# Kernel optimization log

Measured on AMD Instinct MI355X. Metric: run time of the kernel, lower is better.

## Reference

```python
import jax, jax.numpy as jnp
import numpy as np
import math

WIDTH = 1024
NUM_HEADS = 16
HEAD_DIM = WIDTH // NUM_HEADS
WINDOW_SIZE = 256
MIN_LOGITS_VALUE = -1e30


def setup_inputs() -> dict:
    key = jax.random.key(0)
    ks = jax.random.split(key, 7)
    b, t = 2, 2048
    std = math.sqrt(1.0 / WIDTH)
    x = jax.random.normal(ks[0], (b, t, WIDTH), dtype=jnp.float32)
    segment_pos = jnp.broadcast_to(jnp.arange(t, dtype=jnp.int32)[None, :], (b, t))
    Wq = jax.random.normal(ks[1], (WIDTH, WIDTH), dtype=jnp.float32) * std
    Wk = jax.random.normal(ks[2], (HEAD_DIM, WIDTH), dtype=jnp.float32) * std
    Wv = jax.random.normal(ks[3], (HEAD_DIM, WIDTH), dtype=jnp.float32) * std
    Wf = jax.random.normal(ks[4], (WIDTH, WIDTH), dtype=jnp.float32) * std
    bf = jnp.zeros((WIDTH,), dtype=jnp.float32)
    return {"x": x, "segment_pos": segment_pos, "Wq": Wq, "Wk": Wk, "Wv": Wv, "Wf": Wf, "bf": bf}


def reference(x, segment_pos, Wq, Wk, Wv, Wf, bf):
    b, t, _ = x.shape
    # projections (Linear: x @ W.T)
    q = (x @ Wq.T).reshape(b, t, NUM_HEADS, HEAD_DIM)  # [b,t,n,h]
    k = x @ Wk.T  # [b,t,h] single shared KV head (MQA)
    v = x @ Wv.T  # [b,t,h]
    scale = 1.0 / math.sqrt(HEAD_DIM)
    logits = jnp.einsum('btnh,bsh->bnts', q, k) * scale  # [b,n,t,s]
    # sliding-window causal mask: q_pos >= k_pos and q_pos <= k_pos + window
    ar = jnp.arange(t)
    qp = ar[:, None]
    kp = ar[None, :]
    mask = (qp >= kp) & (qp <= kp + WINDOW_SIZE)  # [t,s]
    masked = jnp.where(mask[None, None, :, :], logits, MIN_LOGITS_VALUE)
    probs = jax.nn.softmax(masked.astype(jnp.float32), axis=-1).astype(logits.dtype)
    out = jnp.einsum('bnts,bsh->btnh', probs, v)  # [b,t,n,h]
    out = out.reshape(b, t, WIDTH)
    return out @ Wf.T + bf
```

## Files before the change

### kernel.cpp

```cpp
#include <hip/hip_runtime.h>
#include <stdint.h>

#define B_SZ   2
#define T_SEQ  2048
#define WIDTH_ 1024
#define NH     16
#define HD     64
#define WIN    256
#define MROWS  (B_SZ * T_SEQ)
#define NQKV   1152

typedef __attribute__((ext_vector_type(4))) float f32x4;
typedef __attribute__((ext_vector_type(8))) short s16x8;

typedef __attribute__((address_space(1))) const void gas_void;
typedef __attribute__((address_space(3))) void las_void;

#define MFMA(a, b, c) __builtin_amdgcn_mfma_f32_16x16x32_bf16((a), (b), (c), 0, 0, 0)

__device__ __forceinline__ void gload_lds16(const void* g, void* l) {
  __builtin_amdgcn_global_load_lds((gas_void*)g, (las_void*)l, 16, 0, 0);
}

__device__ __forceinline__ ushort f2bf(float f) {
  union { float f; uint32_t u; } v; v.f = f;
  uint32_t u = v.u;
  return (ushort)((u + 0x7FFFu + ((u >> 16) & 1u)) >> 16);
}

__global__ void prep_kernel(const float* __restrict__ x,
                            const float* __restrict__ Wq,
                            const float* __restrict__ Wk,
                            const float* __restrict__ Wv,
                            const float* __restrict__ Wf,
                            ushort* __restrict__ xb,
                            ushort* __restrict__ wqkv,
                            ushort* __restrict__ wfb) {
  const int XN = MROWS * WIDTH_ / 4;
  const int WQ = NQKV * WIDTH_ / 4;
  const int WF = WIDTH_ * WIDTH_ / 4;
  int i = blockIdx.x * blockDim.x + threadIdx.x;
  float4 v;
  ushort* dst;
  if (i < XN) {
    v = ((const float4*)x)[i];
    dst = xb + i * 4;
  } else if (i < XN + WQ) {
    int j = i - XN;
    int row = (j * 4) >> 10;
    int col = (j * 4) & 1023;
    const float* src = (row < 1024) ? (Wq + row * 1024 + col)
                     : (row < 1088) ? (Wk + (row - 1024) * 1024 + col)
                                    : (Wv + (row - 1088) * 1024 + col);
    v = *(const float4*)src;
    dst = wqkv + j * 4;
  } else if (i < XN + WQ + WF) {
    int j = i - XN - WQ;
    v = ((const float4*)Wf)[j];
    dst = wfb + j * 4;
  } else {
    return;
  }
  ushort4 o;
  o.x = f2bf(v.x); o.y = f2bf(v.y); o.z = f2bf(v.z); o.w = f2bf(v.w);
  *(ushort4*)dst = o;
}

#define G_STAGE(AS, BS, KOFF) do {                                          \
  _Pragma("unroll")                                                         \
  for (int i_ = 0; i_ < 2; ++i_) {                                          \
    int c_ = i_ * 256 + w * 64 + lane;                                      \
    int row_ = c_ >> 2;                                                     \
    int ke_ = (c_ & 3) * 8;                                                 \
    int ldsb_ = (i_ * 256 + w * 64) * 16;                                   \
    gload_lds16(A + (size_t)(m0 + row_) * 1024 + (KOFF) + ke_,              \
                (char*)(AS) + ldsb_);                                       \
    gload_lds16(B + (size_t)(n0 + row_) * 1024 + (KOFF) + ke_,              \
                (char*)(BS) + ldsb_);                                       \
  }                                                                         \
} while (0)

#define G_COMPUTE(AS, BS) do {                                              \
  s16x8 af_[4], bf_[4];                                                     \
  _Pragma("unroll")                                                         \
  for (int t_ = 0; t_ < 4; ++t_) {                                          \
    af_[t_] = *(const s16x8*)&(AS)[(wm + t_ * 16 + r16) * 32 + g * 8];      \
    bf_[t_] = *(const s16x8*)&(BS)[(wn + t_ * 16 + r16) * 32 + g * 8];      \
  }                                                                         \
  _Pragma("unroll")                                                         \
  for (int mb_ = 0; mb_ < 4; ++mb_)                                         \
    _Pragma("unroll")                                                       \
    for (int nb_ = 0; nb_ < 4; ++nb_)                                       \
      acc[mb_][nb_] = MFMA(af_[mb_], bf_[nb_], acc[mb_][nb_]);              \
} while (0)

template <int MODE>
__global__ __launch_bounds__(256) void gemm_kernel(
    const ushort* __restrict__ A, const ushort* __restrict__ B,
    ushort* __restrict__ qb, ushort* __restrict__ kb, ushort* __restrict__ vt,
    float* __restrict__ Cf, const float* __restrict__ bias) {
  const int w = threadIdx.x >> 6;
  const int lane = threadIdx.x & 63;
  const int g = lane >> 4;
  const int r16 = lane & 15;
  const int m0 = blockIdx.y * 128;
  const int n0 = blockIdx.x * 128;
  const int wm = (w >> 1) * 64;
  const int wn = (w & 1) * 64;

  __shared__ ushort As0[128 * 32];
  __shared__ ushort Bs0[128 * 32];
  __shared__ ushort As1[128 * 32];
  __shared__ ushort Bs1[128 * 32];

  f32x4 acc[4][4] = {};

  G_STAGE(As0, Bs0, 0);
  for (int k0 = 0; k0 < 1024; k0 += 64) {
    __syncthreads();
    G_STAGE(As1, Bs1, k0 + 32);
    G_COMPUTE(As0, Bs0);
    __syncthreads();
    if (k0 + 64 < 1024) G_STAGE(As0, Bs0, k0 + 64);
    G_COMPUTE(As1, Bs1);
  }

#pragma unroll
  for (int mb = 0; mb < 4; ++mb)
#pragma unroll
    for (int nb = 0; nb < 4; ++nb) {
      int n = n0 + wn + nb * 16 + r16;
      int mbase = m0 + wm + mb * 16 + 4 * g;
      if (MODE == 0) {
#pragma unroll
        for (int r = 0; r < 4; ++r) {
          ushort h = f2bf(acc[mb][nb][r]);
          int m = mbase + r;
          if (n < 1024)      qb[m * 1024 + n] = h;
          else if (n < 1088) kb[m * 64 + (n - 1024)] = h;
          else               vt[((size_t)((m >> 11) * 64 + (n - 1088))) * 2048 +
                                (m & 2047)] = h;
        }
      } else {
        float bv = bias[n];
#pragma unroll
        for (int r = 0; r < 4; ++r)
          Cf[(size_t)(mbase + r) * 1024 + n] = acc[mb][nb][r] + bv;
      }
    }
}

__global__ __launch_bounds__(64) void attn_kernel(
    const ushort* __restrict__ qb, const ushort* __restrict__ kb,
    const ushort* __restrict__ vt, ushort* __restrict__ ao) {
  const int lane = threadIdx.x;
  const int g = lane >> 4;
  const int r16 = lane & 15;
  const int blk = blockIdx.x;
  const int qt = blk & 63;
  const int h = (blk >> 6) & 15;
  const int b = blk >> 10;
  const int q0 = qt * 32;
  const int qpA = q0 + r16;
  const int qpB = q0 + 16 + r16;

  const ushort* qrowA = qb + (size_t)(b * 2048 + qpA) * 1024 + h * 64;
  const ushort* qrowB = qb + (size_t)(b * 2048 + qpB) * 1024 + h * 64;
  s16x8 qfA0 = *(const s16x8*)(qrowA + g * 8);
  s16x8 qfA1 = *(const s16x8*)(qrowA + 32 + g * 8);
  s16x8 qfB0 = *(const s16x8*)(qrowB + g * 8);
  s16x8 qfB1 = *(const s16x8*)(qrowB + 32 + g * 8);

  f32x4 oaccA[4] = {}, oaccB[4] = {};
  float mA = -1e30f, lA = 0.f, mB = -1e30f, lB = 0.f;

  int kt0 = q0 - WIN;
  if (kt0 < 0) kt0 = 0;
  kt0 &= ~31;

  s16x8 k00, k01, k10, k11;
  {
    const ushort* kp0 = kb + (size_t)(b * 2048 + kt0 + r16) * 64;
    const ushort* kp1 = kb + (size_t)(b * 2048 + kt0 + 16 + r16) * 64;
    k00 = *(const s16x8*)(kp0 + g * 8);
    k01 = *(const s16x8*)(kp0 + 32 + g * 8);
    k10 = *(const s16x8*)(kp1 + g * 8);
    k11 = *(const s16x8*)(kp1 + 32 + g * 8);
  }

  for (int kt = kt0; kt <= q0; kt += 32) {
    s16x8 c00 = k00, c01 = k01, c10 = k10, c11 = k11;
    if (kt + 32 <= q0) {
      const ushort* kp0 = kb + (size_t)(b * 2048 + kt + 32 + r16) * 64;
      const ushort* kp1 = kb + (size_t)(b * 2048 + kt + 48 + r16) * 64;
      k00 = *(const s16x8*)(kp0 + g * 8);
      k01 = *(const s16x8*)(kp0 + 32 + g * 8);
      k10 = *(const s16x8*)(kp1 + g * 8);
      k11 = *(const s16x8*)(kp1 + 32 + g * 8);
    }

    f32x4 sA0 = {}, sA1 = {}, sB0 = {}, sB1 = {};
    sA0 = MFMA(c00, qfA0, sA0); sA0 = MFMA(c01, qfA1, sA0);
    sA1 = MFMA(c10, qfA0, sA1); sA1 = MFMA(c11, qfA1, sA1);
    sB0 = MFMA(c00, qfB0, sB0); sB0 = MFMA(c01, qfB1, sB0);
    sB1 = MFMA(c10, qfB0, sB1); sB1 = MFMA(c11, qfB1, sB1);

    float pA0[4], pA1[4], pB0[4], pB1[4];
    float tmA = -1e30f, tmB = -1e30f;
#pragma unroll
    for (int r = 0; r < 4; ++r) {
      int ka = kt + 4 * g + r;
      int kc = ka + 16;
      float a0 = (ka <= qpA && qpA - ka <= WIN) ? sA0[r] * 0.125f : -1e30f;
      float a1 = (kc <= qpA && qpA - kc <= WIN) ? sA1[r] * 0.125f : -1e30f;
      float b0 = (ka <= qpB && qpB - ka <= WIN) ? sB0[r] * 0.125f : -1e30f;
      float b1 = (kc <= qpB && qpB - kc <= WIN) ? sB1[r] * 0.125f : -1e30f;
      pA0[r] = a0; pA1[r] = a1; pB0[r] = b0; pB1[r] = b1;
      tmA = fmaxf(tmA, fmaxf(a0, a1));
      tmB = fmaxf(tmB, fmaxf(b0, b1));
    }
    tmA = fmaxf(tmA, __shfl_xor(tmA, 16));
    tmA = fmaxf(tmA, __shfl_xor(tmA, 32));
    tmB = fmaxf(tmB, __shfl_xor(tmB, 16));
    tmB = fmaxf(tmB, __shfl_xor(tmB, 32));

    float mnA = fmaxf(mA, tmA), mnB = fmaxf(mB, tmB);
    float corrA = __expf(mA - mnA), corrB = __expf(mB - mnB);
    float tsA = 0.f, tsB = 0.f;
    s16x8 pfA, pfB;
#pragma unroll
    for (int r = 0; r < 4; ++r) {
      float eA0 = __expf(pA0[r] - mnA);
      float eA1 = __expf(pA1[r] - mnA);
      float eB0 = __expf(pB0[r] - mnB);
      float eB1 = __expf(pB1[r] - mnB);
      tsA += eA0 + eA1; tsB += eB0 + eB1;
      pfA[r] = (short)f2bf(eA0); pfA[4 + r] = (short)f2bf(eA1);
      pfB[r] = (short)f2bf(eB0); pfB[4 + r] = (short)f2bf(eB1);
    }
    tsA += __shfl_xor(tsA, 16); tsA += __shfl_xor(tsA, 32);
    tsB += __shfl_xor(tsB, 16); tsB += __shfl_xor(tsB, 32);
    lA = lA * corrA + tsA; mA = mnA;
    lB = lB * corrB + tsB; mB = mnB;

#pragma unroll
    for (int db = 0; db < 4; ++db) { oaccA[db] *= corrA; oaccB[db] *= corrB; }

#pragma unroll
    for (int db = 0; db < 4; ++db) {
      const ushort* vrow = vt + (size_t)(b * 64 + db * 16 + r16) * 2048 + kt;
      ushort4 va = *(const ushort4*)(vrow + 4 * g);
      ushort4 vc = *(const ushort4*)(vrow + 16 + 4 * g);
      s16x8 vf;
      vf[0] = (short)va.x; vf[1] = (short)va.y; vf[2] = (short)va.z; vf[3] = (short)va.w;
      vf[4] = (short)vc.x; vf[5] = (short)vc.y; vf[6] = (short)vc.z; vf[7] = (short)vc.w;
      oaccA[db] = MFMA(vf, pfA, oaccA[db]);
      oaccB[db] = MFMA(vf, pfB, oaccB[db]);
    }
  }

  float invA = 1.0f / lA, invB = 1.0f / lB;
  ushort* orowA = ao + (size_t)(b * 2048 + qpA) * 1024 + h * 64;
  ushort* orowB = ao + (size_t)(b * 2048 + qpB) * 1024 + h * 64;
#pragma unroll
  for (int db = 0; db < 4; ++db) {
    ushort4 oA, oB;
    oA.x = f2bf(oaccA[db][0] * invA); oA.y = f2bf(oaccA[db][1] * invA);
    oA.z = f2bf(oaccA[db][2] * invA); oA.w = f2bf(oaccA[db][3] * invA);
    oB.x = f2bf(oaccB[db][0] * invB); oB.y = f2bf(oaccB[db][1] * invB);
    oB.z = f2bf(oaccB[db][2] * invB); oB.w = f2bf(oaccB[db][3] * invB);
    *(ushort4*)(orowA + db * 16 + 4 * g) = oA;
    *(ushort4*)(orowB + db * 16 + 4 * g) = oB;
  }
}

extern "C" void kernel_launch(void* const* d_in, const int* in_sizes, int n_in,
                              void* d_out, int out_size, void* d_ws, size_t ws_size,
                              hipStream_t stream) {
  const float* x  = (const float*)d_in[0];
  const float* Wq = (const float*)d_in[2];
  const float* Wk = (const float*)d_in[3];
  const float* Wv = (const float*)d_in[4];
  const float* Wf = (const float*)d_in[5];
  const float* bf = (const float*)d_in[6];
  float* out = (float*)d_out;

  uint8_t* w8 = (uint8_t*)d_ws;
  ushort* xb   = (ushort*)(w8 + 0);
  ushort* qbuf = (ushort*)(w8 + 8388608);
  ushort* attn = (ushort*)(w8 + 16777216);
  ushort* wqkv = (ushort*)(w8 + 25165824);
  ushort* wfb  = (ushort*)(w8 + 27525120);
  ushort* kbuf = (ushort*)(w8 + 29622272);
  ushort* vt   = (ushort*)(w8 + 30146560);

  prep_kernel<<<6272, 256, 0, stream>>>(x, Wq, Wk, Wv, Wf, xb, wqkv, wfb);
  gemm_kernel<0><<<dim3(9, 32), 256, 0, stream>>>(xb, wqkv, qbuf, kbuf, vt,
                                                  nullptr, nullptr);
  attn_kernel<<<2048, 64, 0, stream>>>(qbuf, kbuf, vt, attn);
  gemm_kernel<1><<<dim3(8, 32), 256, 0, stream>>>(attn, wfb, nullptr, nullptr,
                                                  nullptr, out, bf);
}
```

Before: 158.6 us.

## Shrink GEMM tiles to 64x64 with XCD swizzle, hoist V loads and set MFMA priority

The GEMM tile shrinks from 128x128 to 64x64 and uses a 1D grid whose block index is remapped across the 8 XCDs. This is meant to give the small M=4096 GEMMs enough workgroups to fill the device. An explicit vmcnt(0) wait is added before each barrier so the global-to-LDS loads are complete before use. In attention, the V fragments are loaded at the top of each iteration so their latency overlaps the QK MFMAs and softmax, and s_setprio brackets the MFMA blocks. Smaller tiles reduce data reuse per block and double global traffic per FLOP.

```diff
diff --git a/kernel.cpp b/kernel.cpp
--- a/kernel.cpp
+++ b/kernel.cpp
@@ -17,6 +17,8 @@
 typedef __attribute__((address_space(3))) void las_void;
 
 #define MFMA(a, b, c) __builtin_amdgcn_mfma_f32_16x16x32_bf16((a), (b), (c), 0, 0, 0)
+
+#define VMEM_DRAIN() asm volatile("s_waitcnt vmcnt(0)" ::: "memory")
 
 __device__ __forceinline__ void gload_lds16(const void* g, void* l) {
   __builtin_amdgcn_global_load_lds((gas_void*)g, (las_void*)l, 16, 0, 0);
@@ -67,30 +69,27 @@
 }
 
 #define G_STAGE(AS, BS, KOFF) do {                                          \
+  int c_ = w * 64 + lane;                                       \
+  int row_ = c_ >> 2;                                                       \
+  int ke_ = (c_ & 3) * 8;                                                   \
+  int ldsb_ = c_ * 16;                     \
+  gload_lds16(A + (size_t)(m0 + row_) * 1024 + (KOFF) + ke_,                \
+              (char*)(AS) + ldsb_);                                         \
+  gload_lds16(B + (size_t)(n0 + row_) * 1024 + (KOFF) + ke_,                \
+              (char*)(BS) + ldsb_);                                         \
+} while (0)
+
+#define G_COMPUTE(AS, BS) do {                                              \
+  s16x8 af_[2], bf_[2];                                                     \
   _Pragma("unroll")                                                         \
-  for (int i_ = 0; i_ < 2; ++i_) {                                          \
-    int c_ = i_ * 256 + w * 64 + lane;                                      \
-    int row_ = c_ >> 2;                                                     \
-    int ke_ = (c_ & 3) * 8;                                                 \
-    int ldsb_ = (i_ * 256 + w * 64) * 16;                                   \
-    gload_lds16(A + (size_t)(m0 + row_) * 1024 + (KOFF) + ke_,              \
-                (char*)(AS) + ldsb_);                                       \
-    gload_lds16(B + (size_t)(n0 + row_) * 1024 + (KOFF) + ke_,              \
-                (char*)(BS) + ldsb_);                                       \
-  }                                                                         \
-} while (0)
-
-#define G_COMPUTE(AS, BS) do {                                              \
-  s16x8 af_[4], bf_[4];                                                     \
-  _Pragma("unroll")                                                         \
-  for (int t_ = 0; t_ < 4; ++t_) {                                          \
+  for (int t_ = 0; t_ < 2; ++t_) {                                          \
     af_[t_] = *(const s16x8*)&(AS)[(wm + t_ * 16 + r16) * 32 + g * 8];      \
     bf_[t_] = *(const s16x8*)&(BS)[(wn + t_ * 16 + r16) * 32 + g * 8];      \
   }                                                                         \
   _Pragma("unroll")                                                         \
-  for (int mb_ = 0; mb_ < 4; ++mb_)                                         \
+  for (int mb_ = 0; mb_ < 2; ++mb_)                                         \
     _Pragma("unroll")                                                       \
-    for (int nb_ = 0; nb_ < 4; ++nb_)                                       \
+    for (int nb_ = 0; nb_ < 2; ++nb_)                                       \
       acc[mb_][nb_] = MFMA(af_[mb_], bf_[nb_], acc[mb_][nb_]);              \
 } while (0)
 
@@ -99,36 +98,45 @@
     const ushort* __restrict__ A, const ushort* __restrict__ B,
     ushort* __restrict__ qb, ushort* __restrict__ kb, ushort* __restrict__ vt,
     float* __restrict__ Cf, const float* __restrict__ bias) {
+  const int NBX = (MODE == 0) ? 18 : 16;
+  const int nwg = NBX * 64;
+  const int cpx = nwg >> 3;
+  int swz = (blockIdx.x & 7) * cpx + (blockIdx.x >> 3);
+  const int bx = swz % NBX;
+  const int by = swz / NBX;
+
   const int w = threadIdx.x >> 6;
   const int lane = threadIdx.x & 63;
   const int g = lane >> 4;
   const int r16 = lane & 15;
-  const int m0 = blockIdx.y * 128;
-  const int n0 = blockIdx.x * 128;
-  const int wm = (w >> 1) * 64;
-  const int wn = (w & 1) * 64;
-
-  __shared__ ushort As0[128 * 32];
-  __shared__ ushort Bs0[128 * 32];
-  __shared__ ushort As1[128 * 32];
-  __shared__ ushort Bs1[128 * 32];
-
-  f32x4 acc[4][4] = {};
+  const int m0 = by * 64;
+  const int n0 = bx * 64;
+  const int wm = (w >> 1) * 32;
+  const int wn = (w & 1) * 32;
+
+  __shared__ ushort As0[64 * 32];
+  __shared__ ushort Bs0[64 * 32];
+  __shared__ ushort As1[64 * 32];
+  __shared__ ushort Bs1[64 * 32];
+
+  f32x4 acc[2][2] = {};
 
   G_STAGE(As0, Bs0, 0);
   for (int k0 = 0; k0 < 1024; k0 += 64) {
+    VMEM_DRAIN();
     __syncthreads();
     G_STAGE(As1, Bs1, k0 + 32);
     G_COMPUTE(As0, Bs0);
+    VMEM_DRAIN();
     __syncthreads();
     if (k0 + 64 < 1024) G_STAGE(As0, Bs0, k0 + 64);
     G_COMPUTE(As1, Bs1);
   }
 
 #pragma unroll
-  for (int mb = 0; mb < 4; ++mb)
-#pragma unroll
-    for (int nb = 0; nb < 4; ++nb) {
+  for (int mb = 0; mb < 2; ++mb)
+#pragma unroll
+    for (int nb = 0; nb < 2; ++nb) {
       int n = n0 + wn + nb * 16 + r16;
       int mbase = m0 + wm + mb * 16 + 4 * g;
       if (MODE == 0) {
@@ -190,6 +198,18 @@
 
   for (int kt = kt0; kt <= q0; kt += 32) {
     s16x8 c00 = k00, c01 = k01, c10 = k10, c11 = k11;
+
+    s16x8 vfr[4];
+#pragma unroll
+    for (int db = 0; db < 4; ++db) {
+      const ushort* vrow = vt + (size_t)(b * 64 + db * 16 + r16) * 2048 + kt;
+      uint2 va = *(const uint2*)(vrow + 4 * g);
+      uint2 vc = *(const uint2*)(vrow + 16 + 4 * g);
+      union { s16x8 v; uint32_t d[4]; } u;
+      u.d[0] = va.x; u.d[1] = va.y; u.d[2] = vc.x; u.d[3] = vc.y;
+      vfr[db] = u.v;
+    }
+
     if (kt + 32 <= q0) {
       const ushort* kp0 = kb + (size_t)(b * 2048 + kt + 32 + r16) * 64;
       const ushort* kp1 = kb + (size_t)(b * 2048 + kt + 48 + r16) * 64;
@@ -200,10 +220,12 @@
     }
 
     f32x4 sA0 = {}, sA1 = {}, sB0 = {}, sB1 = {};
+    __builtin_amdgcn_s_setprio(1);
     sA0 = MFMA(c00, qfA0, sA0); sA0 = MFMA(c01, qfA1, sA0);
     sA1 = MFMA(c10, qfA0, sA1); sA1 = MFMA(c11, qfA1, sA1);
     sB0 = MFMA(c00, qfB0, sB0); sB0 = MFMA(c01, qfB1, sB0);
     sB1 = MFMA(c10, qfB0, sB1); sB1 = MFMA(c11, qfB1, sB1);
+    __builtin_amdgcn_s_setprio(0);
 
     float pA0[4], pA1[4], pB0[4], pB1[4];
     float tmA = -1e30f, tmB = -1e30f;
@@ -246,17 +268,13 @@
 #pragma unroll
     for (int db = 0; db < 4; ++db) { oaccA[db] *= corrA; oaccB[db] *= corrB; }
 
+    __builtin_amdgcn_s_setprio(1);
 #pragma unroll
     for (int db = 0; db < 4; ++db) {
-      const ushort* vrow = vt + (size_t)(b * 64 + db * 16 + r16) * 2048 + kt;
-      ushort4 va = *(const ushort4*)(vrow + 4 * g);
-      ushort4 vc = *(const ushort4*)(vrow + 16 + 4 * g);
-      s16x8 vf;
-      vf[0] = (short)va.x; vf[1] = (short)va.y; vf[2] = (short)va.z; vf[3] = (short)va.w;
-      vf[4] = (short)vc.x; vf[5] = (short)vc.y; vf[6] = (short)vc.z; vf[7] = (short)vc.w;
-      oaccA[db] = MFMA(vf, pfA, oaccA[db]);
-      oaccB[db] = MFMA(vf, pfB, oaccB[db]);
-    }
+      oaccA[db] = MFMA(vfr[db], pfA, oaccA[db]);
+      oaccB[db] = MFMA(vfr[db], pfB, oaccB[db]);
+    }
+    __builtin_amdgcn_s_setprio(0);
   }
 
   float invA = 1.0f / lA, invB = 1.0f / lB;
@@ -295,9 +313,9 @@
   ushort* vt   = (ushort*)(w8 + 30146560);
 
   prep_kernel<<<6272, 256, 0, stream>>>(x, Wq, Wk, Wv, Wf, xb, wqkv, wfb);
-  gemm_kernel<0><<<dim3(9, 32), 256, 0, stream>>>(xb, wqkv, qbuf, kbuf, vt,
-                                                  nullptr, nullptr);
+  gemm_kernel<0><<<1152, 256, 0, stream>>>(xb, wqkv, qbuf, kbuf, vt,
+                                           nullptr, nullptr);
   attn_kernel<<<2048, 64, 0, stream>>>(qbuf, kbuf, vt, attn);
-  gemm_kernel<1><<<dim3(8, 32), 256, 0, stream>>>(attn, wfb, nullptr, nullptr,
-                                                  nullptr, out, bf);
-}
+  gemm_kernel<1><<<1024, 256, 0, stream>>>(attn, wfb, nullptr, nullptr,
+                                           nullptr, out, bf);
+}
```

Result: faster. 153.9 us (-3.0%).
